# Kernel optimization log

Hardware: AMD Instinct MI355X
Metric: run time of the kernel (lower is better)

The kernel has to match this reference:

```python
import jax, jax.numpy as jnp
import numpy as np
from jax import lax

H, W = 512, 1024
C = 34          # Cityscapes label ids; thing classes are 24..33 per Threshold(23.99,50) + <=33
K = 200         # top_k centers kept by NMS
KS = 7          # NMS max-pool kernel
THRESH = 0.1    # NMS score threshold


def setup_inputs() -> dict:
    key = jax.random.key(0)
    k1, k2, k3 = jax.random.split(key, 3)
    return {
        "segmentation_probs": jax.random.normal(k1, (2, C, H, W), jnp.float32),
        "center_maps": jax.random.uniform(k2, (2, 1, H, W), jnp.float32),
        "regression_maps": jax.random.normal(k3, (2, 2, H, W), jnp.float32) * 8.0,
    }


def _nms(center_maps):
    # MaxPool2d(KS, stride=1, pad=KS//2) -> Threshold(0.1, 0) -> keep only local maxima
    pad = KS // 2
    pooled = lax.reduce_window(center_maps, -jnp.inf, lax.max,
                               (1, 1, KS, KS), (1, 1, 1, 1),
                               [(0, 0), (0, 0), (pad, pad), (pad, pad)])
    thresholded = jnp.where(pooled > THRESH, pooled, 0.0)
    # torch: center_map[thresholded != center_map] = 0
    nms_map = jnp.where(thresholded == center_maps, center_maps, 0.0)[:, 0]  # (B,H,W)
    # padded equivalent of nonzero + argsort(desc) + [:top_k]
    probs, idx = lax.top_k(nms_map.reshape(nms_map.shape[0], -1), K)          # (B,K)
    ys, xs = idx // W, idx % W
    return ys, xs, probs, probs > 0.0


def _per_sample(args):
    seg, seg_probs, reg, ys, xs, probs, valid = args
    # --- CreateInstMap: brute-force center-distance argmin ---
    px = (jnp.arange(W, dtype=jnp.float32) + 1.0)[None, :] - reg[0]   # (H,W) pred center x
    py = (jnp.arange(H, dtype=jnp.float32) + 1.0)[:, None] - reg[1]   # (H,W) pred center y
    dx = px[:, :, None] - xs.astype(jnp.float32)[None, None, :]       # (H,W,K)
    dy = py[:, :, None] - ys.astype(jnp.float32)[None, None, :]
    dist2 = dx * dx + dy * dy            # argmin(sqrt(d2)) == argmin(d2); sqrt omitted safely
    dist2 = jnp.where(valid[None, None, :], dist2, jnp.inf)           # ignore padded centers
    closest = jnp.argmin(dist2, -1).astype(jnp.int32) + 1             # (H,W), ids in 1..K
    # --- SeperateInstMap: thing mask, per-instance majority class / mean prob ---
    things = (seg >= 24) & (seg <= 33)   # Threshold(23.99,50) then <= 33
    inst_ids = jnp.where(things, closest, 0)                          # 0 = background/stuff
    flat_ids = inst_ids.reshape(-1)
    comb = flat_ids * C + seg.reshape(-1)                             # joint (inst, class) id
    counts = jax.ops.segment_sum(jnp.ones(H * W, jnp.float32), comb,
                                 num_segments=(K + 1) * C).reshape(K + 1, C)[1:]   # (K,C)
    sums = jax.ops.segment_sum(seg_probs.reshape(C, -1).T, flat_ids,
                               num_segments=K + 1)[1:]                # (K,C) prob sums per inst
    n = counts.sum(-1)                                                # (K,) pixels per instance
    inst_class = jnp.argmax(counts, -1).astype(jnp.int32)             # majority seg class
    s = jnp.take_along_axis(sums, inst_class[:, None], axis=1)[:, 0]
    seg_prob = jnp.where(n > 0, s / jnp.maximum(n, 1.0), 0.0)         # mean seg prob over mask
    return inst_class, probs, seg_prob, n.astype(jnp.int32), (n > 0) & valid, closest


def reference(segmentation_probs, center_maps, regression_maps):
    seg_probs = jax.nn.softmax(segmentation_probs, axis=1)
    segs = jnp.argmax(segmentation_probs, axis=1).astype(jnp.int32)   # (B,H,W)
    ys, xs, probs, valid = _nms(center_maps)
    # sequential over batch (mirrors python loop, bounds peak memory of (H,W,K) field)
    inst_class, inst_prob, seg_prob, n_pix, valid_inst, closest = lax.map(
        _per_sample, (segs, seg_probs, regression_maps, ys, xs, probs, valid))
    return inst_class, inst_prob, seg_prob, n_pix, valid_inst, segs, closest
```

## Files before the change

### kernel.cpp

```cpp
#include <hip/hip_runtime.h>
#include <stdint.h>

#define NB 2
#define NC 34
#define HH 512
#define WW 1024
#define HWW (HH*WW)
#define KK 200
#define MCAP 4096
#define VBIN 4096
#define SLOTS 256
#define NTILE 256
#define CAP2 32768
#define SEGB (NB*HWW/1024)
#define NMSB (NB*NTILE)

#define TW 128
#define TH 16
#define HALO 3

__global__ void __launch_bounds__(256)
k_seg_nms(const float* __restrict__ logits, const float* __restrict__ cmap,
          float* __restrict__ segs_out, float* __restrict__ scomb,
          unsigned char* __restrict__ seg8,
          uint64_t* __restrict__ cand, uint32_t* __restrict__ tcnt,
          uint32_t* __restrict__ counts, float* __restrict__ sums,
          uint32_t* __restrict__ cnt, uint32_t* __restrict__ ghist,
          int use_stats) {
    int bid = blockIdx.x;
    int tid = threadIdx.x;

    if (bid < SEGB) {
        if (bid == 0) {
            for (int i = tid; i < NB * (KK + 1) * NC; i += 256) counts[i] = 0u;
            for (int i = tid; i < NB * (KK + 1); i += 256) sums[i] = 0.f;
            for (int i = tid; i < NB * VBIN; i += 256) ghist[i] = 0u;
            if (tid < NB) cnt[tid] = 0u;
        }
        int t = bid * 256 + tid;
        int p = t * 4;
        int b = p / HWW, r = p - b * HWW;
        const float* base = logits + (size_t)b * NC * HWW + r;
        float4 m = make_float4(-3e38f, -3e38f, -3e38f, -3e38f);
        float4 s = make_float4(0.f, 0.f, 0.f, 0.f);
        int ax = 0, ay = 0, az = 0, aw = 0;
#pragma unroll
        for (int c = 0; c < NC; ++c) {
            float4 v = *(const float4*)(base + (size_t)c * HWW);
            if (v.x > m.x) { s.x = s.x * __expf(m.x - v.x) + 1.f; m.x = v.x; ax = c; }
            else            s.x += __expf(v.x - m.x);
            if (v.y > m.y) { s.y = s.y * __expf(m.y - v.y) + 1.f; m.y = v.y; ay = c; }
            else            s.y += __expf(v.y - m.y);
            if (v.z > m.z) { s.z = s.z * __expf(m.z - v.z) + 1.f; m.z = v.z; az = c; }
            else            s.z += __expf(v.z - m.z);
            if (v.w > m.w) { s.w = s.w * __expf(m.w - v.w) + 1.f; m.w = v.w; aw = c; }
            else            s.w += __expf(v.w - m.w);
        }
        *(float4*)(segs_out + p) = make_float4((float)ax, (float)ay, (float)az, (float)aw);
        *(uchar4*)(seg8 + p) = make_uchar4((unsigned char)ax, (unsigned char)ay,
                                           (unsigned char)az, (unsigned char)aw);
        if (use_stats) {
            *(float4*)(scomb + p) = make_float4(m.x + __logf(s.x), m.y + __logf(s.y),
                                                m.z + __logf(s.z), m.w + __logf(s.w));
        }
        return;
    }

    __shared__ float sIn[TH + 2 * HALO][TW + 2 * HALO];
    __shared__ float sH[TH + 2 * HALO][TW];
    __shared__ uint64_t lc[SLOTS];
    __shared__ uint32_t lcnt;
    int t2 = bid - SEGB;
    int bx = t2 & (WW / TW - 1);
    int by = (t2 >> 3) & (HH / TH - 1);
    int b = t2 >> 8;
    int tb = t2 & (NTILE - 1);
    const float* bb = cmap + (size_t)b * HWW;
    if (tid == 0) lcnt = 0u;

    const int LW = TW + 2 * HALO;
    const int LH = TH + 2 * HALO;
    for (int idx = tid; idx < LW * LH; idx += 256) {
        int r = idx / LW, c = idx - r * LW;
        int gh = by * TH + r - HALO;
        int gw = bx * TW + c - HALO;
        float v = -3e38f;
        if (gh >= 0 && gh < HH && gw >= 0 && gw < WW) v = bb[gh * WW + gw];
        sIn[r][c] = v;
    }
    __syncthreads();
    for (int idx = tid; idx < LH * TW; idx += 256) {
        int r = idx / TW, c = idx - r * TW;
        float m = fmaxf(fmaxf(fmaxf(sIn[r][c], sIn[r][c + 1]),
                              fmaxf(sIn[r][c + 2], sIn[r][c + 3])),
                        fmaxf(fmaxf(sIn[r][c + 4], sIn[r][c + 5]), sIn[r][c + 6]));
        sH[r][c] = m;
    }
    __syncthreads();
    for (int idx = tid; idx < TH * TW; idx += 256) {
        int r = idx >> 7, c = idx & (TW - 1);
        float cv = sIn[r + HALO][c + HALO];
        float m = fmaxf(fmaxf(fmaxf(sH[r][c], sH[r + 1][c]),
                              fmaxf(sH[r + 2][c], sH[r + 3][c])),
                        fmaxf(fmaxf(sH[r + 4][c], sH[r + 5][c]), sH[r + 6][c]));
        if (m > 0.1f && cv == m) {
            int gh = by * TH + r;
            int gw = bx * TW + c;
            uint32_t rr = (uint32_t)(gh * WW + gw);
            uint32_t pos = atomicAdd(&lcnt, 1u);
            if (pos < SLOTS)
                lc[pos] = ((uint64_t)__float_as_uint(cv) << 32) |
                          (uint64_t)(0xFFFFFFFFu - rr);
        }
    }
    __syncthreads();
    uint32_t n = lcnt;
    if (n > SLOTS) n = SLOTS;
    uint64_t* cslot = cand + ((size_t)(b * NTILE + tb)) * SLOTS;
    for (uint32_t i = tid; i < n; i += 256) cslot[i] = lc[i];
    if (tid == 0) tcnt[b * NTILE + tb] = n;
}

__global__ void __launch_bounds__(256) k_compact(const uint64_t* __restrict__ cand,
                                                 const uint32_t* __restrict__ tcnt,
                                                 uint64_t* __restrict__ cand2,
                                                 uint32_t* __restrict__ cnt,
                                                 uint32_t* __restrict__ ghist) {
    __shared__ uint64_t lc2[2048];
    __shared__ uint32_t lcnt, gbase;
    __shared__ uint32_t ltc8[8];
    int bid = blockIdx.x;
    int b = bid >> 5;
    int chunk = bid & 31;
    int tid = threadIdx.x;
    if (tid == 0) lcnt = 0u;
    if (tid < 8) ltc8[tid] = tcnt[b * NTILE + chunk * 8 + tid];
    __syncthreads();
    const uint64_t* cb = cand + ((size_t)b * NTILE + chunk * 8) * SLOTS;
#pragma unroll
    for (int it = 0; it < 8; ++it) {
        int idx = it * 256 + tid;
        int tile = idx >> 8, sl = idx & 255;
        if ((uint32_t)sl < ltc8[tile]) {
            uint64_t kk = cb[idx];
            uint32_t pos = atomicAdd(&lcnt, 1u);
            lc2[pos] = kk;
            float v = __uint_as_float((uint32_t)(kk >> 32));
            int bin = (int)(v * (float)VBIN);
            bin = bin < 0 ? 0 : (bin > VBIN - 1 ? VBIN - 1 : bin);
            atomicAdd(&ghist[b * VBIN + bin], 1u);
        }
    }
    __syncthreads();
    uint32_t m = lcnt;
    if (tid == 0 && m) gbase = atomicAdd(&cnt[b], m);
    __syncthreads();
    for (uint32_t i = tid; i < m; i += 256) {
        uint32_t pos = gbase + i;
        if (pos < CAP2) cand2[(size_t)b * CAP2 + pos] = lc2[i];
    }
}

__global__ void __launch_bounds__(1024) k_topk2(const uint64_t* __restrict__ cand2,
                                                const uint32_t* __restrict__ cnt,
                                                const uint32_t* __restrict__ ghist,
                                                float* __restrict__ probs_out,
                                                float* __restrict__ cxy) {
    int b = blockIdx.x;
    int tid = threadIdx.x;
    int lane = tid & 63, wv = tid >> 6;
    __shared__ uint32_t hist[VBIN];
    __shared__ uint32_t part[1024];
    __shared__ uint32_t wsum[16];
    __shared__ uint64_t lkey[MCAP];
    __shared__ uint32_t lM;
    __shared__ int sBstar;

    if (tid < KK) {
        probs_out[b * KK + tid] = 0.f;
        cxy[(b * KK + tid) * 2]     = 1e19f;
        cxy[(b * KK + tid) * 2 + 1] = 1e19f;
    }
    if (tid == 0) { lM = 0u; sBstar = 0; }
    for (int i = tid; i < VBIN; i += 1024) hist[i] = ghist[b * VBIN + i];
    uint32_t N = cnt[b];
    if (N > CAP2) N = CAP2;
    const uint64_t* cb = cand2 + (size_t)b * CAP2;
    __syncthreads();

    int base = VBIN - 4 * (tid + 1);
    uint32_t s = hist[base] + hist[base + 1] + hist[base + 2] + hist[base + 3];
    uint32_t sc = s;
#pragma unroll
    for (int off = 1; off < 64; off <<= 1) {
        uint32_t nv = __shfl_up(sc, off, 64);
        if (lane >= off) sc += nv;
    }
    if (lane == 63) wsum[wv] = sc;
    __syncthreads();
    if (wv == 0) {
        uint32_t t0 = (lane < 16) ? wsum[lane] : 0u;
#pragma unroll
        for (int off = 1; off < 16; off <<= 1) {
            uint32_t nv = __shfl_up(t0, off, 64);
            if (lane >= off) t0 += nv;
        }
        if (lane < 16) wsum[lane] = t0;
    }
    __syncthreads();
    uint32_t inc = sc + (wv > 0 ? wsum[wv - 1] : 0u);
    part[tid] = inc;
    __syncthreads();
    {
        uint32_t Pt = part[tid];
        uint32_t Pp = (tid > 0) ? part[tid - 1] : 0u;
        if (Pt >= KK && Pp < KK) {
            uint32_t cum = Pp;
            int bs = base;
            for (int j = base + 3; j >= base; --j) {
                cum += hist[j];
                if (cum >= KK) { bs = j; break; }
            }
            sBstar = bs;
        }
    }
    __syncthreads();
    int bstar = sBstar;

    for (uint32_t i = tid; i < N; i += 1024) {
        uint64_t kk = cb[i];
        float v = __uint_as_float((uint32_t)(kk >> 32));
        int bin = (int)(v * (float)VBIN);
        bin = bin < 0 ? 0 : (bin > VBIN - 1 ? VBIN - 1 : bin);
        if (bin >= bstar) {
            uint32_t pos = atomicAdd(&lM, 1u);
            if (pos < MCAP) lkey[pos] = kk;
        }
    }
    __syncthreads();
    uint32_t M = lM;
    if (M > MCAP) M = MCAP;
    for (uint32_t i = tid; i < M; i += 1024) {
        uint64_t kk = lkey[i];
        uint32_t rank = 0;
        for (uint32_t j = 0; j < M; ++j) rank += (lkey[j] > kk) ? 1u : 0u;
        if (rank < KK) {
            uint32_t bits = (uint32_t)(kk >> 32);
            uint32_t idx = 0xFFFFFFFFu - (uint32_t)(kk & 0xFFFFFFFFull);
            probs_out[b * KK + rank] = __uint_as_float(bits);
            cxy[(b * KK + rank) * 2]     = (float)(idx % WW);
            cxy[(b * KK + rank) * 2 + 1] = (float)(idx / WW);
        }
    }
}

__global__ void __launch_bounds__(256) k_assign(const float* __restrict__ reg,
                                                const float* __restrict__ cxy,
                                                const unsigned char* __restrict__ seg8,
                                                float* __restrict__ closest_out,
                                                uint16_t* __restrict__ aux,
                                                uint32_t* __restrict__ counts) {
    __shared__ float2 cc[KK];
    __shared__ float4 ccs[KK];
    __shared__ float sred[4][4];
    __shared__ uint32_t wcnt[4];
    __shared__ float stau2;
    __shared__ uint32_t sS;

    int t = blockIdx.x;
    int tx = t & 63;
    int ty = (t >> 6) & 31;
    int b = t >> 11;
    int tid = threadIdx.x;
    int lane = tid & 63, wv = tid >> 6;
    int w = tx * 16 + (tid & 15);
    int h = ty * 16 + (tid >> 4);
    int r = h * WW + w;
    int p = b * HWW + r;

    if (tid < KK) cc[tid] = ((const float2*)cxy)[b * KK + tid];
    __syncthreads();

    float rx = reg[(size_t)b * 2 * HWW + r];
    float ry = reg[(size_t)b * 2 * HWW + HWW + r];
    float px = (float)(w + 1) - rx;
    float py = (float)(h + 1) - ry;

    float mnx = px, mxx = px, mny = py, mxy = py;
#pragma unroll
    for (int off = 1; off < 64; off <<= 1) {
        mnx = fminf(mnx, __shfl_xor(mnx, off, 64));
        mxx = fmaxf(mxx, __shfl_xor(mxx, off, 64));
        mny = fminf(mny, __shfl_xor(mny, off, 64));
        mxy = fmaxf(mxy, __shfl_xor(mxy, off, 64));
    }
    if (lane == 0) { sred[0][wv] = mnx; sred[1][wv] = mxx; sred[2][wv] = mny; sred[3][wv] = mxy; }
    __syncthreads();
    float xmin = fminf(fminf(sred[0][0], sred[0][1]), fminf(sred[0][2], sred[0][3]));
    float xmax = fmaxf(fmaxf(sred[1][0], sred[1][1]), fmaxf(sred[1][2], sred[1][3]));
    float ymin = fminf(fminf(sred[2][0], sred[2][1]), fminf(sred[2][2], sred[2][3]));
    float ymax = fmaxf(fmaxf(sred[3][0], sred[3][1]), fmaxf(sred[3][2], sred[3][3]));

    float2 c0 = cc[tid < KK ? tid : 0];
    float mdx = fmaxf(fmaxf(xmin - c0.x, c0.x - xmax), 0.f);
    float mdy = fmaxf(fmaxf(ymin - c0.y, c0.y - ymax), 0.f);
    float mind2 = mdx * mdx + mdy * mdy;
    float Mdx = fmaxf(c0.x - xmin, xmax - c0.x);
    float Mdy = fmaxf(c0.y - ymin, ymax - c0.y);
    float maxd2 = Mdx * Mdx + Mdy * Mdy;

    float v = (tid < KK) ? maxd2 : 3.0e38f;
#pragma unroll
    for (int off = 1; off < 64; off <<= 1) v = fminf(v, __shfl_xor(v, off, 64));
    if (lane == 0) sred[0][wv] = v;
    __syncthreads();
    if (tid == 0) {
        float mm = fminf(fminf(sred[0][0], sred[0][1]), fminf(sred[0][2], sred[0][3]));
        float tau = __builtin_sqrtf(mm) + 1.0f;
        stau2 = tau * tau;
    }
    __syncthreads();

    bool flag = (tid < KK) && (mind2 <= stau2);
    uint64_t mask = __ballot(flag);
    uint32_t myoff = (uint32_t)__popcll(mask & ((1ull << lane) - 1ull));
    if (lane == 0) wcnt[wv] = (uint32_t)__popcll(mask);
    __syncthreads();
    uint32_t pre = 0;
    for (int i = 0; i < wv; ++i) pre += wcnt[i];
    if (flag) ccs[pre + myoff] = make_float4(c0.x, c0.y, (float)tid, 0.f);
    if (tid == 0) sS = wcnt[0] + wcnt[1] + wcnt[2] + wcnt[3];
    __syncthreads();
    uint32_t S = sS;

    float best = __builtin_inff();
    float bkf = 0.f;
    for (uint32_t s = 0; s < S; ++s) {
        float4 c = ccs[s];
        float dx = __fsub_rn(px, c.x);
        float dy = __fsub_rn(py, c.y);
        float d2 = __fadd_rn(__fmul_rn(dx, dx), __fmul_rn(dy, dy));
        if (d2 < best) { best = d2; bkf = c.z; }
    }
    int bk = (int)bkf;
    closest_out[p] = bkf + 1.0f;
    int seg = (int)seg8[p];
    aux[p] = (uint16_t)(((bk + 1) << 6) | seg);
    if (seg >= 24 && seg <= 33) {
        atomicAdd(&counts[(b * (KK + 1) + (bk + 1)) * NC + seg], 1u);
    }
}

__global__ void __launch_bounds__(256) k_inst(const uint32_t* __restrict__ counts,
                                              const float* __restrict__ probs_out,
                                              float* __restrict__ ic_out,
                                              float* __restrict__ np_out,
                                              float* __restrict__ va_out) {
    int t = blockIdx.x * 256 + threadIdx.x;
    if (t >= NB * KK) return;
    int b = t / KK, k = t - b * KK;
    const uint32_t* row = counts + (size_t)(b * (KK + 1) + (k + 1)) * NC;
    uint32_t n = 0, mx = 0;
    int am = 0;
#pragma unroll
    for (int c = 0; c < NC; ++c) {
        uint32_t x = row[c];
        n += x;
        if (x > mx) { mx = x; am = c; }
    }
    ic_out[t] = (float)am;
    np_out[t] = (float)n;
    va_out[t] = (n > 0u && probs_out[t] > 0.f) ? 1.f : 0.f;
}

template <int USE_STATS>
__global__ void __launch_bounds__(256) k_sums(const float* __restrict__ logits,
                                              const uint16_t* __restrict__ aux,
                                              const float* __restrict__ scomb,
                                              const float* __restrict__ icf,
                                              float* __restrict__ sums) {
    __shared__ int ic_l[KK];
    __shared__ float psum[KK + 1];
    int tid = threadIdx.x;
    int p0 = blockIdx.x * 512;
    int b = p0 / HWW;
    if (tid < KK) ic_l[tid] = (int)icf[b * KK + tid];
    if (tid < KK + 1) psum[tid] = 0.f;
    __syncthreads();
    int p = p0 + tid * 2;
    int r = p - b * HWW;
    uint32_t a2 = *(const uint32_t*)(aux + p);
    int seg0 = (int)(a2 & 63u), seg1 = (int)((a2 >> 16) & 63u);
    bool th0 = (seg0 >= 24) & (seg0 <= 33);
    bool th1 = (seg1 >= 24) & (seg1 <= 33);
    float2 sc = make_float2(0.f, 0.f);
    if (USE_STATS && (th0 || th1)) sc = *(const float2*)(scomb + p);
    const float* base = logits + (size_t)b * NC * HWW + r;
#pragma unroll
    for (int j = 0; j < 2; ++j) {
        bool th = j ? th1 : th0;
        if (th) {
            uint32_t pk = (a2 >> (16 * j)) & 0xFFFFu;
            int cl = (int)(pk >> 6);
            int ic = ic_l[cl - 1];
            float pr;
            if (USE_STATS) {
                float lv = base[(size_t)ic * HWW + j];
                pr = __expf(lv - (j ? sc.y : sc.x));
            } else {
                float vmax = -3e38f, lv = 0.f, s = 0.f;
                float vv[NC];
#pragma unroll
                for (int c = 0; c < NC; ++c) {
                    vv[c] = base[(size_t)c * HWW + j];
                    vmax = fmaxf(vmax, vv[c]);
                    if (c == ic) lv = vv[c];
                }
#pragma unroll
                for (int c = 0; c < NC; ++c) s += __expf(vv[c] - vmax);
                pr = __expf(lv - vmax) / s;
            }
            atomicAdd(&psum[cl], pr);
        }
    }
    __syncthreads();
    if (tid < KK + 1) {
        float x = psum[tid];
        if (x != 0.f) atomicAdd(&sums[b * (KK + 1) + tid], x);
    }
}

__global__ void __launch_bounds__(256) k_segprob(const float* __restrict__ sums,
                                                 const float* __restrict__ np_out,
                                                 float* __restrict__ sp_out) {
    int t = blockIdx.x * 256 + threadIdx.x;
    if (t >= NB * KK) return;
    int b = t / KK, k = t - b * KK;
    float n = np_out[t];
    float s = sums[b * (KK + 1) + k + 1];
    sp_out[t] = (n > 0.f) ? (s / n) : 0.f;
}

extern "C" void kernel_launch(void* const* d_in, const int* in_sizes, int n_in,
                              void* d_out, int out_size, void* d_ws, size_t ws_size,
                              hipStream_t stream) {
    const float* logits = (const float*)d_in[0];
    const float* cmap   = (const float*)d_in[1];
    const float* reg    = (const float*)d_in[2];
    float* out = (float*)d_out;
    float* o_ic   = out;
    float* o_prob = out + NB * KK;
    float* o_sp   = out + 2 * NB * KK;
    float* o_np   = out + 3 * NB * KK;
    float* o_va   = out + 4 * NB * KK;
    float* o_segs = out + 5 * NB * KK;
    float* o_clo  = out + 5 * NB * KK + NB * HWW;

    char* w = (char*)d_ws;
    size_t off = 0;
    auto alloc = [&](size_t bytes) {
        off = (off + 15) & ~((size_t)15);
        void* p = w + off;
        off += bytes;
        return p;
    };
    uint64_t* cand   = (uint64_t*)alloc(sizeof(uint64_t) * NB * NTILE * SLOTS);
    uint64_t* cand2  = (uint64_t*)alloc(sizeof(uint64_t) * NB * CAP2);
    uint32_t* tcnt   = (uint32_t*)alloc(sizeof(uint32_t) * NB * NTILE);
    uint32_t* cnt    = (uint32_t*)alloc(sizeof(uint32_t) * NB);
    uint32_t* ghist  = (uint32_t*)alloc(sizeof(uint32_t) * NB * VBIN);
    uint32_t* counts = (uint32_t*)alloc(sizeof(uint32_t) * NB * (KK + 1) * NC);
    float* sums      = (float*)alloc(sizeof(float) * NB * (KK + 1));
    float* cxy       = (float*)alloc(sizeof(float) * NB * KK * 2);
    unsigned char* seg8 = (unsigned char*)alloc(sizeof(unsigned char) * NB * HWW);
    uint16_t* aux    = (uint16_t*)alloc(sizeof(uint16_t) * NB * HWW);
    size_t base_need = (off + 15) & ~((size_t)15);
    float* scomb = (float*)(w + base_need);
    int use_stats = (base_need + sizeof(float) * (size_t)NB * HWW) <= ws_size ? 1 : 0;

    k_seg_nms<<<SEGB + NMSB, 256, 0, stream>>>(logits, cmap, o_segs, scomb, seg8,
                                               cand, tcnt, counts, sums, cnt, ghist,
                                               use_stats);
    k_compact<<<NB * 32, 256, 0, stream>>>(cand, tcnt, cand2, cnt, ghist);
    k_topk2<<<NB, 1024, 0, stream>>>(cand2, cnt, ghist, o_prob, cxy);
    k_assign<<<NB * 2048, 256, 0, stream>>>(reg, cxy, seg8, o_clo, aux, counts);
    k_inst<<<(NB * KK + 255) / 256, 256, 0, stream>>>(counts, o_prob, o_ic, o_np, o_va);
    if (use_stats)
        k_sums<1><<<NB * HWW / 512, 256, 0, stream>>>(logits, aux, scomb, o_ic, sums);
    else
        k_sums<0><<<NB * HWW / 512, 256, 0, stream>>>(logits, aux, scomb, o_ic, sums);
    k_segprob<<<(NB * KK + 255) / 256, 256, 0, stream>>>(sums, o_np, o_sp);
}
```

Baseline: 110.7 us.

## Fuse compaction into NMS, fold instance stats into sums kernel, memset workspace

The NMS tiles now append their local maxima straight into the global candidate buffer and update the score histogram themselves, so the separate compaction kernel and its intermediate buffer are gone. The per-instance class and count computation moves into the sums kernel. Each sums block now covers a 4096-pixel strip and recomputes the instance argmax for its own use, and only the first strip of each batch writes it out. Zeroing of the counters moves from block 0 of the first kernel to a single memset, which removes two launches and a race-prone init in exchange for redundant argmax work in every sums block.

After: 113.2 us. +2.2%, slower.

```diff
diff --git a/kernel.cpp b/kernel.cpp
--- a/kernel.cpp
+++ b/kernel.cpp
@@ -14,6 +14,7 @@
 #define CAP2 32768
 #define SEGB (NB*HWW/1024)
 #define NMSB (NB*NTILE)
+#define STRIP 4096
 
 #define TW 128
 #define TH 16
@@ -23,20 +24,12 @@
 k_seg_nms(const float* __restrict__ logits, const float* __restrict__ cmap,
           float* __restrict__ segs_out, float* __restrict__ scomb,
           unsigned char* __restrict__ seg8,
-          uint64_t* __restrict__ cand, uint32_t* __restrict__ tcnt,
-          uint32_t* __restrict__ counts, float* __restrict__ sums,
-          uint32_t* __restrict__ cnt, uint32_t* __restrict__ ghist,
-          int use_stats) {
+          uint64_t* __restrict__ cand2, uint32_t* __restrict__ cnt,
+          uint32_t* __restrict__ ghist, int use_stats) {
     int bid = blockIdx.x;
     int tid = threadIdx.x;
 
     if (bid < SEGB) {
-        if (bid == 0) {
-            for (int i = tid; i < NB * (KK + 1) * NC; i += 256) counts[i] = 0u;
-            for (int i = tid; i < NB * (KK + 1); i += 256) sums[i] = 0.f;
-            for (int i = tid; i < NB * VBIN; i += 256) ghist[i] = 0u;
-            if (tid < NB) cnt[tid] = 0u;
-        }
         int t = bid * 256 + tid;
         int p = t * 4;
         int b = p / HWW, r = p - b * HWW;
@@ -69,12 +62,11 @@
     __shared__ float sIn[TH + 2 * HALO][TW + 2 * HALO];
     __shared__ float sH[TH + 2 * HALO][TW];
     __shared__ uint64_t lc[SLOTS];
-    __shared__ uint32_t lcnt;
+    __shared__ uint32_t lcnt, gbase;
     int t2 = bid - SEGB;
     int bx = t2 & (WW / TW - 1);
     int by = (t2 >> 3) & (HH / TH - 1);
     int b = t2 >> 8;
-    int tb = t2 & (NTILE - 1);
     const float* bb = cmap + (size_t)b * HWW;
     if (tid == 0) lcnt = 0u;
 
@@ -108,56 +100,23 @@
             int gw = bx * TW + c;
             uint32_t rr = (uint32_t)(gh * WW + gw);
             uint32_t pos = atomicAdd(&lcnt, 1u);
-            if (pos < SLOTS)
+            if (pos < SLOTS) {
                 lc[pos] = ((uint64_t)__float_as_uint(cv) << 32) |
                           (uint64_t)(0xFFFFFFFFu - rr);
+                int bin = (int)(cv * (float)VBIN);
+                bin = bin < 0 ? 0 : (bin > VBIN - 1 ? VBIN - 1 : bin);
+                atomicAdd(&ghist[b * VBIN + bin], 1u);
+            }
         }
     }
     __syncthreads();
     uint32_t n = lcnt;
     if (n > SLOTS) n = SLOTS;
-    uint64_t* cslot = cand + ((size_t)(b * NTILE + tb)) * SLOTS;
-    for (uint32_t i = tid; i < n; i += 256) cslot[i] = lc[i];
-    if (tid == 0) tcnt[b * NTILE + tb] = n;
-}
-
-__global__ void __launch_bounds__(256) k_compact(const uint64_t* __restrict__ cand,
-                                                 const uint32_t* __restrict__ tcnt,
-                                                 uint64_t* __restrict__ cand2,
-                                                 uint32_t* __restrict__ cnt,
-                                                 uint32_t* __restrict__ ghist) {
-    __shared__ uint64_t lc2[2048];
-    __shared__ uint32_t lcnt, gbase;
-    __shared__ uint32_t ltc8[8];
-    int bid = blockIdx.x;
-    int b = bid >> 5;
-    int chunk = bid & 31;
-    int tid = threadIdx.x;
-    if (tid == 0) lcnt = 0u;
-    if (tid < 8) ltc8[tid] = tcnt[b * NTILE + chunk * 8 + tid];
-    __syncthreads();
-    const uint64_t* cb = cand + ((size_t)b * NTILE + chunk * 8) * SLOTS;
-#pragma unroll
-    for (int it = 0; it < 8; ++it) {
-        int idx = it * 256 + tid;
-        int tile = idx >> 8, sl = idx & 255;
-        if ((uint32_t)sl < ltc8[tile]) {
-            uint64_t kk = cb[idx];
-            uint32_t pos = atomicAdd(&lcnt, 1u);
-            lc2[pos] = kk;
-            float v = __uint_as_float((uint32_t)(kk >> 32));
-            int bin = (int)(v * (float)VBIN);
-            bin = bin < 0 ? 0 : (bin > VBIN - 1 ? VBIN - 1 : bin);
-            atomicAdd(&ghist[b * VBIN + bin], 1u);
-        }
-    }
-    __syncthreads();
-    uint32_t m = lcnt;
-    if (tid == 0 && m) gbase = atomicAdd(&cnt[b], m);
-    __syncthreads();
-    for (uint32_t i = tid; i < m; i += 256) {
+    if (tid == 0 && n) gbase = atomicAdd(&cnt[b], n);
+    __syncthreads();
+    for (uint32_t i = tid; i < n; i += 256) {
         uint32_t pos = gbase + i;
-        if (pos < CAP2) cand2[(size_t)b * CAP2 + pos] = lc2[i];
+        if (pos < CAP2) cand2[(size_t)b * CAP2 + pos] = lc[i];
     }
 }
 
@@ -351,76 +310,81 @@
     }
 }
 
-__global__ void __launch_bounds__(256) k_inst(const uint32_t* __restrict__ counts,
-                                              const float* __restrict__ probs_out,
-                                              float* __restrict__ ic_out,
-                                              float* __restrict__ np_out,
-                                              float* __restrict__ va_out) {
-    int t = blockIdx.x * 256 + threadIdx.x;
-    if (t >= NB * KK) return;
-    int b = t / KK, k = t - b * KK;
-    const uint32_t* row = counts + (size_t)(b * (KK + 1) + (k + 1)) * NC;
-    uint32_t n = 0, mx = 0;
-    int am = 0;
-#pragma unroll
-    for (int c = 0; c < NC; ++c) {
-        uint32_t x = row[c];
-        n += x;
-        if (x > mx) { mx = x; am = c; }
-    }
-    ic_out[t] = (float)am;
-    np_out[t] = (float)n;
-    va_out[t] = (n > 0u && probs_out[t] > 0.f) ? 1.f : 0.f;
-}
-
 template <int USE_STATS>
 __global__ void __launch_bounds__(256) k_sums(const float* __restrict__ logits,
                                               const uint16_t* __restrict__ aux,
                                               const float* __restrict__ scomb,
-                                              const float* __restrict__ icf,
-                                              float* __restrict__ sums) {
+                                              const uint32_t* __restrict__ counts,
+                                              const float* __restrict__ probs_out,
+                                              float* __restrict__ sums,
+                                              float* __restrict__ ic_out,
+                                              float* __restrict__ np_out,
+                                              float* __restrict__ va_out) {
     __shared__ int ic_l[KK];
     __shared__ float psum[KK + 1];
     int tid = threadIdx.x;
-    int p0 = blockIdx.x * 512;
-    int b = p0 / HWW;
-    if (tid < KK) ic_l[tid] = (int)icf[b * KK + tid];
+    int sblk = blockIdx.x;
+    int b = sblk / (HWW / STRIP);
+    int p0 = sblk * STRIP;
+
+    if (tid < KK) {
+        const uint32_t* row = counts + (size_t)(b * (KK + 1) + (tid + 1)) * NC;
+        uint32_t n = 0, mx = 0;
+        int am = 0;
+#pragma unroll
+        for (int c = 0; c < NC; ++c) {
+            uint32_t x = row[c];
+            n += x;
+            if (x > mx) { mx = x; am = c; }
+        }
+        ic_l[tid] = am;
+        if ((sblk % (HWW / STRIP)) == 0) {
+            ic_out[b * KK + tid] = (float)am;
+            np_out[b * KK + tid] = (float)n;
+            va_out[b * KK + tid] =
+                (n > 0u && probs_out[b * KK + tid] > 0.f) ? 1.f : 0.f;
+        }
+    }
     if (tid < KK + 1) psum[tid] = 0.f;
     __syncthreads();
-    int p = p0 + tid * 2;
-    int r = p - b * HWW;
-    uint32_t a2 = *(const uint32_t*)(aux + p);
-    int seg0 = (int)(a2 & 63u), seg1 = (int)((a2 >> 16) & 63u);
-    bool th0 = (seg0 >= 24) & (seg0 <= 33);
-    bool th1 = (seg1 >= 24) & (seg1 <= 33);
-    float2 sc = make_float2(0.f, 0.f);
-    if (USE_STATS && (th0 || th1)) sc = *(const float2*)(scomb + p);
-    const float* base = logits + (size_t)b * NC * HWW + r;
-#pragma unroll
-    for (int j = 0; j < 2; ++j) {
-        bool th = j ? th1 : th0;
-        if (th) {
-            uint32_t pk = (a2 >> (16 * j)) & 0xFFFFu;
-            int cl = (int)(pk >> 6);
-            int ic = ic_l[cl - 1];
-            float pr;
-            if (USE_STATS) {
-                float lv = base[(size_t)ic * HWW + j];
-                pr = __expf(lv - (j ? sc.y : sc.x));
-            } else {
-                float vmax = -3e38f, lv = 0.f, s = 0.f;
-                float vv[NC];
-#pragma unroll
-                for (int c = 0; c < NC; ++c) {
-                    vv[c] = base[(size_t)c * HWW + j];
-                    vmax = fmaxf(vmax, vv[c]);
-                    if (c == ic) lv = vv[c];
+
+#pragma unroll 1
+    for (int ch = 0; ch < STRIP / 512; ++ch) {
+        int p = p0 + ch * 512 + tid * 2;
+        int r = p - b * HWW;
+        uint32_t a2 = *(const uint32_t*)(aux + p);
+        int seg0 = (int)(a2 & 63u), seg1 = (int)((a2 >> 16) & 63u);
+        bool th0 = (seg0 >= 24) & (seg0 <= 33);
+        bool th1 = (seg1 >= 24) & (seg1 <= 33);
+        float2 sc = make_float2(0.f, 0.f);
+        if (USE_STATS && (th0 || th1)) sc = *(const float2*)(scomb + p);
+        const float* base = logits + (size_t)b * NC * HWW + r;
+#pragma unroll
+        for (int j = 0; j < 2; ++j) {
+            bool th = j ? th1 : th0;
+            if (th) {
+                uint32_t pk = (a2 >> (16 * j)) & 0xFFFFu;
+                int cl = (int)(pk >> 6);
+                int ic = ic_l[cl - 1];
+                float pr;
+                if (USE_STATS) {
+                    float lv = base[(size_t)ic * HWW + j];
+                    pr = __expf(lv - (j ? sc.y : sc.x));
+                } else {
+                    float vmax = -3e38f, lv = 0.f, s = 0.f;
+                    float vv[NC];
+#pragma unroll
+                    for (int c = 0; c < NC; ++c) {
+                        vv[c] = base[(size_t)c * HWW + j];
+                        vmax = fmaxf(vmax, vv[c]);
+                        if (c == ic) lv = vv[c];
+                    }
+#pragma unroll
+                    for (int c = 0; c < NC; ++c) s += __expf(vv[c] - vmax);
+                    pr = __expf(lv - vmax) / s;
                 }
-#pragma unroll
-                for (int c = 0; c < NC; ++c) s += __expf(vv[c] - vmax);
-                pr = __expf(lv - vmax) / s;
+                atomicAdd(&psum[cl], pr);
             }
-            atomicAdd(&psum[cl], pr);
         }
     }
     __syncthreads();
@@ -464,13 +428,14 @@
         off += bytes;
         return p;
     };
-    uint64_t* cand   = (uint64_t*)alloc(sizeof(uint64_t) * NB * NTILE * SLOTS);
+    uint32_t* zbase  = (uint32_t*)alloc(sizeof(uint32_t) * (4 + NB * VBIN + NB * (KK + 1) * NC + NB * (KK + 1)));
+    uint32_t* cnt    = zbase;
+    uint32_t* ghist  = zbase + 4;
+    uint32_t* counts = ghist + NB * VBIN;
+    float*    sums   = (float*)(counts + NB * (KK + 1) * NC);
+    size_t zbytes = sizeof(uint32_t) * (4 + NB * VBIN + NB * (KK + 1) * NC + NB * (KK + 1));
+
     uint64_t* cand2  = (uint64_t*)alloc(sizeof(uint64_t) * NB * CAP2);
-    uint32_t* tcnt   = (uint32_t*)alloc(sizeof(uint32_t) * NB * NTILE);
-    uint32_t* cnt    = (uint32_t*)alloc(sizeof(uint32_t) * NB);
-    uint32_t* ghist  = (uint32_t*)alloc(sizeof(uint32_t) * NB * VBIN);
-    uint32_t* counts = (uint32_t*)alloc(sizeof(uint32_t) * NB * (KK + 1) * NC);
-    float* sums      = (float*)alloc(sizeof(float) * NB * (KK + 1));
     float* cxy       = (float*)alloc(sizeof(float) * NB * KK * 2);
     unsigned char* seg8 = (unsigned char*)alloc(sizeof(unsigned char) * NB * HWW);
     uint16_t* aux    = (uint16_t*)alloc(sizeof(uint16_t) * NB * HWW);
@@ -478,16 +443,16 @@
     float* scomb = (float*)(w + base_need);
     int use_stats = (base_need + sizeof(float) * (size_t)NB * HWW) <= ws_size ? 1 : 0;
 
+    hipMemsetAsync(zbase, 0, zbytes, stream);
     k_seg_nms<<<SEGB + NMSB, 256, 0, stream>>>(logits, cmap, o_segs, scomb, seg8,
-                                               cand, tcnt, counts, sums, cnt, ghist,
-                                               use_stats);
-    k_compact<<<NB * 32, 256, 0, stream>>>(cand, tcnt, cand2, cnt, ghist);
+                                               cand2, cnt, ghist, use_stats);
     k_topk2<<<NB, 1024, 0, stream>>>(cand2, cnt, ghist, o_prob, cxy);
     k_assign<<<NB * 2048, 256, 0, stream>>>(reg, cxy, seg8, o_clo, aux, counts);
-    k_inst<<<(NB * KK + 255) / 256, 256, 0, stream>>>(counts, o_prob, o_ic, o_np, o_va);
     if (use_stats)
-        k_sums<1><<<NB * HWW / 512, 256, 0, stream>>>(logits, aux, scomb, o_ic, sums);
+        k_sums<1><<<NB * HWW / STRIP, 256, 0, stream>>>(logits, aux, scomb, counts,
+                                                        o_prob, sums, o_ic, o_np, o_va);
     else
-        k_sums<0><<<NB * HWW / 512, 256, 0, stream>>>(logits, aux, scomb, o_ic, sums);
+        k_sums<0><<<NB * HWW / STRIP, 256, 0, stream>>>(logits, aux, scomb, counts,
+                                                        o_prob, sums, o_ic, o_np, o_va);
     k_segprob<<<(NB * KK + 255) / 256, 256, 0, stream>>>(sums, o_np, o_sp);
 }
```
